# Optimization experiments

Measured on AMD Instinct MI355X. Metric: run time of the kernel, lower is better.

Reference implementation:

```python
import jax, jax.numpy as jnp
import numpy as np

B, S, N, D = 4, 4, 2048, 2048  # batch, residual streams, seq len, model dim


def rmsnorm(x, gamma, eps=1e-12):
    # F.normalize(x, dim=-1) * sqrt(d) * (gamma + 1)
    n = jnp.sqrt(jnp.sum(x * x, axis=-1, keepdims=True))
    return x / jnp.maximum(n, eps) * (x.shape[-1] ** 0.5) * (gamma + 1.0)


def setup_inputs() -> dict:
    key = jax.random.key(0)
    k0, k1, k2, k3 = jax.random.split(key, 4)
    residuals = jax.random.normal(k0, (B * S, N, D), dtype=jnp.float32)
    gamma = (jax.random.normal(k1, (D,), dtype=jnp.float32) * 0.02)
    # ProjActScale weights are zero-init in the module; use small random values
    # so the dynamic paths are numerically exercised.
    w_alpha = jax.random.normal(k2, (S + 1, D), dtype=jnp.float32) * 0.02
    w_beta = jax.random.normal(k3, (1, D), dtype=jnp.float32) * 0.02
    scale_alpha = jnp.asarray(0.01, dtype=jnp.float32)
    scale_beta = jnp.asarray(0.01, dtype=jnp.float32)
    # static_alpha = cat([init_alpha0, eye(S)], dim=1), layer_index=0 -> one-hot row 0
    init_alpha0 = np.zeros((S, 1), dtype=np.float32)
    init_alpha0[0, 0] = 1.0
    static_alpha = jnp.asarray(np.concatenate([init_alpha0, np.eye(S, dtype=np.float32)], axis=1))
    static_beta = jnp.ones((S,), dtype=jnp.float32)
    return dict(residuals=residuals, gamma=gamma, w_alpha=w_alpha, scale_alpha=scale_alpha,
                static_alpha=static_alpha, w_beta=w_beta, scale_beta=scale_beta,
                static_beta=static_beta)


def reference(residuals, gamma, w_alpha, scale_alpha, static_alpha, w_beta, scale_beta, static_beta):
    bs, n, d = residuals.shape
    s = static_beta.shape[0]
    b = bs // s
    # '(b s) n d -> b n s d'
    x = residuals.reshape(b, s, n, d).transpose(0, 2, 1, 3)
    normed = rmsnorm(x, gamma)
    # dynamic alpha / beta: zero-bias linear -> tanh -> scale
    dyn_alpha = jnp.tanh(jnp.einsum('bnsd,td->bnst', normed, w_alpha)) * scale_alpha
    alpha = dyn_alpha + static_alpha                      # (b, n, s, s+1)
    dyn_beta = jnp.tanh(jnp.einsum('bnsd,od->bnso', normed, w_beta))[..., 0] * scale_beta
    beta = dyn_beta + static_beta                         # (b, n, s)
    # width connection: mix residual streams
    mix = jnp.einsum('bnst,bnsd->bntd', alpha, x)         # (b, n, s+1, d)
    branch_input = mix[:, :, 0, :]                        # (b, n, d)
    res = mix[:, :, 1:, :]                                # (b, n, s, d)
    # identity branch (module has branch=None; the add_residual closure applies this)
    branch_out = branch_input
    # depth connection: outer product with beta, add residuals
    res = branch_out[:, :, None, :] * beta[..., None] + res
    # 'b n s d -> (b s) n d'
    out = res.transpose(0, 2, 1, 3).reshape(bs, n, d)
    return out
```

## Files before the change

### kernel.cpp

```cpp
#include <hip/hip_runtime.h>
#include <math.h>

#define NB 4
#define NS 4
#define NN 2048
#define ND 2048
#define NTHREADS 512
#define SQRT_D 45.254833995939045f

typedef float f32x4 __attribute__((ext_vector_type(4)));

#define SHIP(I, H, M_) {                                      \
    const float keep_ = hi_ ? v[(I)+(H)] : v[(I)];            \
    const float give_ = hi_ ? v[(I)] : v[(I)+(H)];            \
    v[(I)] = keep_ + __shfl_xor(give_, (M_)); }

__global__ __launch_bounds__(NTHREADS, 4)
void hyperconn_kernel(const float* __restrict__ residuals,
                      const float* __restrict__ gamma,
                      const float* __restrict__ w_alpha,
                      const float* __restrict__ scale_alpha,
                      const float* __restrict__ static_alpha,
                      const float* __restrict__ w_beta,
                      const float* __restrict__ scale_beta,
                      const float* __restrict__ static_beta,
                      float* __restrict__ out)
{
    __shared__ float red[8][32];
    __shared__ float asb[NS][6];

    const int tid  = threadIdx.x;
    const int bn   = blockIdx.x;
    const int b    = bn >> 11;
    const int n    = bn & (NN - 1);
    const int wave = tid >> 6;
    const int lane = tid & 63;
    const int d    = tid << 2;

    const size_t row_stride = (size_t)NN * ND;
    const float* xp = residuals + (size_t)(b * NS) * row_stride + (size_t)n * ND + d;
    float*       op = out       + (size_t)(b * NS) * row_stride + (size_t)n * ND + d;

    f32x4 x0 = *(const f32x4*)(xp);
    f32x4 x1 = *(const f32x4*)(xp + row_stride);
    f32x4 x2 = *(const f32x4*)(xp + 2 * row_stride);
    f32x4 x3 = *(const f32x4*)(xp + 3 * row_stride);

    float v[32];
#pragma unroll
    for (int k = 0; k < 32; ++k) v[k] = 0.f;

    {
        f32x4 g4 = *(const f32x4*)(gamma + d);
#pragma unroll
        for (int e = 0; e < 4; ++e) {
            v[0]  = __builtin_fmaf(x0[e], x0[e], v[0]);
            v[7]  = __builtin_fmaf(x1[e], x1[e], v[7]);
            v[14] = __builtin_fmaf(x2[e], x2[e], v[14]);
            v[21] = __builtin_fmaf(x3[e], x3[e], v[21]);
        }
#pragma unroll
        for (int j = 0; j < 6; ++j) {
            const float* wsrc = (j < 5) ? (w_alpha + (size_t)j * ND + d)
                                        : (w_beta + d);
            f32x4 w4 = *(const f32x4*)wsrc;
            f32x4 wg = w4 + w4 * g4;
#pragma unroll
            for (int e = 0; e < 4; ++e) {
                v[1 + j]  = __builtin_fmaf(x0[e], wg[e], v[1 + j]);
                v[8 + j]  = __builtin_fmaf(x1[e], wg[e], v[8 + j]);
                v[15 + j] = __builtin_fmaf(x2[e], wg[e], v[15 + j]);
                v[22 + j] = __builtin_fmaf(x3[e], wg[e], v[22 + j]);
            }
        }
    }

    { const bool hi_ = (lane & 1) != 0;
      SHIP(0,16,1)  SHIP(1,16,1)  SHIP(2,16,1)  SHIP(3,16,1)
      SHIP(4,16,1)  SHIP(5,16,1)  SHIP(6,16,1)  SHIP(7,16,1)
      SHIP(8,16,1)  SHIP(9,16,1)  SHIP(10,16,1) SHIP(11,16,1)
      SHIP(12,16,1) SHIP(13,16,1) SHIP(14,16,1) SHIP(15,16,1) }
    { const bool hi_ = (lane & 2) != 0;
      SHIP(0,8,2) SHIP(1,8,2) SHIP(2,8,2) SHIP(3,8,2)
      SHIP(4,8,2) SHIP(5,8,2) SHIP(6,8,2) SHIP(7,8,2) }
    { const bool hi_ = (lane & 4) != 0;
      SHIP(0,4,4) SHIP(1,4,4) SHIP(2,4,4) SHIP(3,4,4) }
    { const bool hi_ = (lane & 8) != 0;
      SHIP(0,2,8) SHIP(1,2,8) }
    { const bool hi_ = (lane & 16) != 0;
      SHIP(0,1,16) }
    const float tot = v[0] + __shfl_xor(v[0], 32);
    const int idx = ((lane & 1) << 4) | ((lane & 2) << 2) | (lane & 4)
                  | ((lane & 8) >> 2) | ((lane & 16) >> 4);
    if (lane < 32) red[wave][idx] = tot;
    __syncthreads();

    if (tid < 24) {
        const int s = tid / 6;
        const int j = tid % 6;
        float ssq = 0.f, dot = 0.f;
#pragma unroll
        for (int w = 0; w < 8; ++w) {
            ssq += red[w][s * 7];
            dot += red[w][s * 7 + 1 + j];
        }
        const float rs = SQRT_D / fmaxf(sqrtf(ssq), 1e-12f);
        const float th = tanhf(dot * rs);
        asb[s][j] = (j < 5) ? (th * scale_alpha[0] + static_alpha[s * 5 + j])
                            : (th * scale_beta[0]  + static_beta[s]);
    }
    __syncthreads();

    float M[NS][NS];
#pragma unroll
    for (int so = 0; so < NS; ++so)
#pragma unroll
        for (int si = 0; si < NS; ++si)
            M[so][si] = __builtin_fmaf(asb[so][5], asb[si][0], asb[si][so + 1]);

#pragma unroll
    for (int so = 0; so < NS; ++so) {
        f32x4 o;
#pragma unroll
        for (int e = 0; e < 4; ++e)
            o[e] = M[so][0] * x0[e] + M[so][1] * x1[e]
                 + M[so][2] * x2[e] + M[so][3] * x3[e];
        __builtin_nontemporal_store(o, (f32x4*)(op + (size_t)so * row_stride));
    }
}

extern "C" void kernel_launch(void* const* d_in, const int* in_sizes, int n_in,
                              void* d_out, int out_size, void* d_ws, size_t ws_size,
                              hipStream_t stream) {
    const float* residuals    = (const float*)d_in[0];
    const float* gamma        = (const float*)d_in[1];
    const float* w_alpha      = (const float*)d_in[2];
    const float* scale_alpha  = (const float*)d_in[3];
    const float* static_alpha = (const float*)d_in[4];
    const float* w_beta       = (const float*)d_in[5];
    const float* scale_beta   = (const float*)d_in[6];
    const float* static_beta  = (const float*)d_in[7];
    float* out = (float*)d_out;

    const int grid = NB * NN;
    hyperconn_kernel<<<grid, NTHREADS, 0, stream>>>(
        residuals, gamma, w_alpha, scale_alpha, static_alpha,
        w_beta, scale_beta, static_beta, out);
}
```

Baseline: 82.78 us.

## Assign one wave per token row and reduce entirely with shuffles

Each wave now owns a whole (b,n) row, looping over the model dimension in 8 chunks, so the cross-wave shared-memory reduction and both __syncthreads barriers are replaced by wave-level shuffles. The mixing coefficients are computed and broadcast inside the wave. In exchange, the residual row is read twice (once for the reductions and once for the mix), relying on cache hits for the second pass, and each wave processes a longer serial loop. Blocks shrink to 256 threads holding four rows each.

```diff
diff --git a/kernel.cpp b/kernel.cpp
--- a/kernel.cpp
+++ b/kernel.cpp
@@ -5,7 +5,7 @@
 #define NS 4
 #define NN 2048
 #define ND 2048
-#define NTHREADS 512
+#define NTHREADS 256
 #define SQRT_D 45.254833995939045f
 
 typedef float f32x4 __attribute__((ext_vector_type(4)));
@@ -14,6 +14,25 @@
     const float keep_ = hi_ ? v[(I)+(H)] : v[(I)];            \
     const float give_ = hi_ ? v[(I)] : v[(I)+(H)];            \
     v[(I)] = keep_ + __shfl_xor(give_, (M_)); }
+
+#define BUTTERFLY()                                                          \
+    { const bool hi_ = (lane & 1) != 0;                                      \
+      SHIP(0,16,1)  SHIP(1,16,1)  SHIP(2,16,1)  SHIP(3,16,1)                 \
+      SHIP(4,16,1)  SHIP(5,16,1)  SHIP(6,16,1)  SHIP(7,16,1)                 \
+      SHIP(8,16,1)  SHIP(9,16,1)  SHIP(10,16,1) SHIP(11,16,1)                \
+      SHIP(12,16,1) SHIP(13,16,1) SHIP(14,16,1) SHIP(15,16,1) }              \
+    { const bool hi_ = (lane & 2) != 0;                                      \
+      SHIP(0,8,2) SHIP(1,8,2) SHIP(2,8,2) SHIP(3,8,2)                        \
+      SHIP(4,8,2) SHIP(5,8,2) SHIP(6,8,2) SHIP(7,8,2) }                      \
+    { const bool hi_ = (lane & 4) != 0;                                      \
+      SHIP(0,4,4) SHIP(1,4,4) SHIP(2,4,4) SHIP(3,4,4) }                      \
+    { const bool hi_ = (lane & 8) != 0;                                      \
+      SHIP(0,2,8) SHIP(1,2,8) }                                              \
+    { const bool hi_ = (lane & 16) != 0;                                     \
+      SHIP(0,1,16) }
+
+#define BREV5(k) ((((k) & 1) << 4) | (((k) & 2) << 2) | ((k) & 4) \
+                | (((k) & 8) >> 2) | (((k) & 16) >> 4))
 
 __global__ __launch_bounds__(NTHREADS, 4)
 void hyperconn_kernel(const float* __restrict__ residuals,
@@ -26,31 +45,36 @@
                       const float* __restrict__ static_beta,
                       float* __restrict__ out)
 {
-    __shared__ float red[8][32];
-    __shared__ float asb[NS][6];
-
     const int tid  = threadIdx.x;
-    const int bn   = blockIdx.x;
+    const int wave = tid >> 6;
+    const int lane = tid & 63;
+    const int bn   = blockIdx.x * 4 + wave;
     const int b    = bn >> 11;
     const int n    = bn & (NN - 1);
-    const int wave = tid >> 6;
-    const int lane = tid & 63;
-    const int d    = tid << 2;
+    const int dl   = lane << 2;
 
     const size_t row_stride = (size_t)NN * ND;
-    const float* xp = residuals + (size_t)(b * NS) * row_stride + (size_t)n * ND + d;
-    float*       op = out       + (size_t)(b * NS) * row_stride + (size_t)n * ND + d;
+    const float* xw = residuals + (size_t)(b * NS) * row_stride + (size_t)n * ND;
+    float*       ow = out       + (size_t)(b * NS) * row_stride + (size_t)n * ND;
 
-    f32x4 x0 = *(const f32x4*)(xp);
-    f32x4 x1 = *(const f32x4*)(xp + row_stride);
-    f32x4 x2 = *(const f32x4*)(xp + 2 * row_stride);
-    f32x4 x3 = *(const f32x4*)(xp + 3 * row_stride);
+    const float sa = scale_alpha[0], sb = scale_beta[0];
+    const int l24 = (lane < 24) ? lane : 0;
+    const int es = l24 / 6, ej = l24 % 6;
+    const float stat = (ej < 5) ? static_alpha[es * 5 + ej] : static_beta[es];
+    const int src_ssq = BREV5(es * 7);
+    const int src_dot = BREV5(es * 7 + 1 + ej);
 
     float v[32];
 #pragma unroll
     for (int k = 0; k < 32; ++k) v[k] = 0.f;
 
-    {
+#pragma unroll
+    for (int c = 0; c < 8; ++c) {
+        const int d = c * 256 + dl;
+        f32x4 x0 = *(const f32x4*)(xw + d);
+        f32x4 x1 = *(const f32x4*)(xw + row_stride + d);
+        f32x4 x2 = *(const f32x4*)(xw + 2 * row_stride + d);
+        f32x4 x3 = *(const f32x4*)(xw + 3 * row_stride + d);
         f32x4 g4 = *(const f32x4*)(gamma + d);
 #pragma unroll
         for (int e = 0; e < 4; ++e) {
@@ -75,57 +99,42 @@
         }
     }
 
-    { const bool hi_ = (lane & 1) != 0;
-      SHIP(0,16,1)  SHIP(1,16,1)  SHIP(2,16,1)  SHIP(3,16,1)
-      SHIP(4,16,1)  SHIP(5,16,1)  SHIP(6,16,1)  SHIP(7,16,1)
-      SHIP(8,16,1)  SHIP(9,16,1)  SHIP(10,16,1) SHIP(11,16,1)
-      SHIP(12,16,1) SHIP(13,16,1) SHIP(14,16,1) SHIP(15,16,1) }
-    { const bool hi_ = (lane & 2) != 0;
-      SHIP(0,8,2) SHIP(1,8,2) SHIP(2,8,2) SHIP(3,8,2)
-      SHIP(4,8,2) SHIP(5,8,2) SHIP(6,8,2) SHIP(7,8,2) }
-    { const bool hi_ = (lane & 4) != 0;
-      SHIP(0,4,4) SHIP(1,4,4) SHIP(2,4,4) SHIP(3,4,4) }
-    { const bool hi_ = (lane & 8) != 0;
-      SHIP(0,2,8) SHIP(1,2,8) }
-    { const bool hi_ = (lane & 16) != 0;
-      SHIP(0,1,16) }
+    BUTTERFLY()
     const float tot = v[0] + __shfl_xor(v[0], 32);
-    const int idx = ((lane & 1) << 4) | ((lane & 2) << 2) | (lane & 4)
-                  | ((lane & 8) >> 2) | ((lane & 16) >> 4);
-    if (lane < 32) red[wave][idx] = tot;
-    __syncthreads();
 
-    if (tid < 24) {
-        const int s = tid / 6;
-        const int j = tid % 6;
-        float ssq = 0.f, dot = 0.f;
+    const float ssq = __shfl(tot, src_ssq);
+    const float dot = __shfl(tot, src_dot);
+    const float rs  = SQRT_D / fmaxf(sqrtf(ssq), 1e-12f);
+    const float aval = __builtin_fmaf(tanhf(dot * rs), (ej < 5) ? sa : sb, stat);
+
+    float a0[4];
 #pragma unroll
-        for (int w = 0; w < 8; ++w) {
-            ssq += red[w][s * 7];
-            dot += red[w][s * 7 + 1 + j];
-        }
-        const float rs = SQRT_D / fmaxf(sqrtf(ssq), 1e-12f);
-        const float th = tanhf(dot * rs);
-        asb[s][j] = (j < 5) ? (th * scale_alpha[0] + static_alpha[s * 5 + j])
-                            : (th * scale_beta[0]  + static_beta[s]);
+    for (int si = 0; si < 4; ++si) a0[si] = __shfl(aval, si * 6);
+    float M[4][4];
+#pragma unroll
+    for (int so = 0; so < 4; ++so) {
+        const float bso = __shfl(aval, so * 6 + 5);
+#pragma unroll
+        for (int si = 0; si < 4; ++si)
+            M[so][si] = __builtin_fmaf(bso, a0[si], __shfl(aval, si * 6 + so + 1));
     }
-    __syncthreads();
-
-    float M[NS][NS];
-#pragma unroll
-    for (int so = 0; so < NS; ++so)
-#pragma unroll
-        for (int si = 0; si < NS; ++si)
-            M[so][si] = __builtin_fmaf(asb[so][5], asb[si][0], asb[si][so + 1]);
 
 #pragma unroll
-    for (int so = 0; so < NS; ++so) {
-        f32x4 o;
+    for (int c = 0; c < 8; ++c) {
+        const int d = c * 256 + dl;
+        f32x4 y0 = *(const f32x4*)(xw + d);
+        f32x4 y1 = *(const f32x4*)(xw + row_stride + d);
+        f32x4 y2 = *(const f32x4*)(xw + 2 * row_stride + d);
+        f32x4 y3 = *(const f32x4*)(xw + 3 * row_stride + d);
 #pragma unroll
-        for (int e = 0; e < 4; ++e)
-            o[e] = M[so][0] * x0[e] + M[so][1] * x1[e]
-                 + M[so][2] * x2[e] + M[so][3] * x3[e];
-        __builtin_nontemporal_store(o, (f32x4*)(op + (size_t)so * row_stride));
+        for (int so = 0; so < 4; ++so) {
+            f32x4 o;
+#pragma unroll
+            for (int e = 0; e < 4; ++e)
+                o[e] = M[so][0] * y0[e] + M[so][1] * y1[e]
+                     + M[so][2] * y2[e] + M[so][3] * y3[e];
+            __builtin_nontemporal_store(o, (f32x4*)(ow + (size_t)so * row_stride + d));
+        }
     }
 }
 
@@ -142,7 +151,7 @@
     const float* static_beta  = (const float*)d_in[7];
     float* out = (float*)d_out;
 
-    const int grid = NB * NN;
+    const int grid = NB * NN / 4;
     hyperconn_kernel<<<grid, NTHREADS, 0, stream>>>(
         residuals, gamma, w_alpha, scale_alpha, static_alpha,
         w_beta, scale_beta, static_beta, out);
```

After: 153.6 us. +85.5%, slower.
